# Kernel tuning notes

Measured on AMD Instinct MI355X. Metric: run time of the kernel, lower is better.

Reference implementation:

```python
import jax, jax.numpy as jnp
import numpy as np

B, L, D, C, H, NB = 2, 2048, 256, 8, 8, 2
S = 2                        # spatial coord dim of s
E = 2 * D - (C + 1)          # id-embedding width per D*2-(C+1)
FIN = 1 + S + E + C          # z + s + id-embed + conditionals
MAXLOC = 4096
DH = (2 * D) // H            # per-head dim


def _ln(x, sc, b):
    m = x.mean(-1, keepdims=True)
    v = ((x - m) ** 2).mean(-1, keepdims=True)
    return (x - m) * jax.lax.rsqrt(v + 1e-6) * sc + b


def setup_inputs() -> dict:
    key = jax.random.key(0)
    ks = iter(jax.random.split(key, 64))
    nrm = lambda shape: jax.random.normal(next(ks), shape, jnp.float32) * 0.02
    inp = {
        "z": jax.random.normal(next(ks), (B, L), jnp.float32),
        "conditionals": jax.random.normal(next(ks), (C,), jnp.float32),
        "s": jax.random.uniform(next(ks), (L, S), jnp.float32),
        "K": jax.random.uniform(next(ks), (L, L), jnp.float32),
        "embed": nrm((MAXLOC, E)),
        "W_in1": nrm((FIN, 4 * D)), "b_in1": jnp.zeros((4 * D,), jnp.float32),
        "W_in2": nrm((4 * D, D)), "b_in2": jnp.zeros((D,), jnp.float32),
        "bias_w": jnp.ones((NB,), jnp.float32), "bias_b": jnp.zeros((NB,), jnp.float32),
        "Wq": nrm((NB, D, 2 * D)), "bq": jnp.zeros((NB, 2 * D), jnp.float32),
        "Wk": nrm((NB, D, 2 * D)), "bk": jnp.zeros((NB, 2 * D), jnp.float32),
        "Wv": nrm((NB, D, 2 * D)), "bv": jnp.zeros((NB, 2 * D), jnp.float32),
        "Wo": nrm((NB, 2 * D, D)), "bo": jnp.zeros((NB, D), jnp.float32),
        "ln1_s": jnp.ones((NB, D), jnp.float32), "ln1_b": jnp.zeros((NB, D), jnp.float32),
        "ln2_s": jnp.ones((NB, D), jnp.float32), "ln2_b": jnp.zeros((NB, D), jnp.float32),
        "Wf1": nrm((NB, D, 4 * D)), "bf1": jnp.zeros((NB, 4 * D), jnp.float32),
        "Wf2": nrm((NB, 4 * D, D)), "bf2": jnp.zeros((NB, D), jnp.float32),
        "Wh1": nrm((D, 128)), "bh1": jnp.zeros((128,), jnp.float32),
        "Wh2": nrm((128, 1)), "bh2": jnp.zeros((1,), jnp.float32),
    }
    return inp


def reference(z, conditionals, s, K, embed, W_in1, b_in1, W_in2, b_in2,
              bias_w, bias_b, Wq, bq, Wk, bk, Wv, bv, Wo, bo,
              ln1_s, ln1_b, ln2_s, ln2_b, Wf1, bf1, Wf2, bf2,
              Wh1, bh1, Wh2, bh2):
    Bx, Lx = z.shape
    ids_e = embed[:Lx]  # ids = arange(L), so embedding lookup is a leading slice
    feats = jnp.concatenate([
        z[..., None],                                          # (B, L, 1)
        jnp.broadcast_to(s[None], (Bx, Lx, S)),                # (B, L, S)
        jnp.broadcast_to(ids_e[None], (Bx, Lx, E)),            # (B, L, E)
        jnp.broadcast_to(conditionals[None, None], (Bx, Lx, C)),  # cond_as_feats
    ], axis=-1)
    x = jax.nn.gelu(feats @ W_in1 + b_in1) @ W_in2 + b_in2     # (B, L, D)
    for i in range(NB):
        bias = bias_w[i] * K + bias_b[i]                        # learned scalar-affine kernel bias (L, L)
        h = _ln(x, ln1_s[i], ln1_b[i])
        q = (h @ Wq[i] + bq[i]).reshape(Bx, Lx, H, DH)
        k = (h @ Wk[i] + bk[i]).reshape(Bx, Lx, H, DH)
        v = (h @ Wv[i] + bv[i]).reshape(Bx, Lx, H, DH)
        scores = jnp.einsum('bqhd,bkhd->bhqk', q, k) / jnp.sqrt(jnp.float32(DH))
        scores = scores + bias[None, None]                      # broadcast over batch, heads
        a = jax.nn.softmax(scores, axis=-1)
        o = jnp.einsum('bhqk,bkhd->bqhd', a, v).reshape(Bx, Lx, 2 * D)
        x = x + (o @ Wo[i] + bo[i])
        h2 = _ln(x, ln2_s[i], ln2_b[i])
        x = x + jax.nn.gelu(h2 @ Wf1[i] + bf1[i]) @ Wf2[i] + bf2[i]
    return jax.nn.gelu(x @ Wh1 + bh1) @ Wh2 + bh2              # head MLP([128,1]) -> (B, L, 1)
```

## Files before the change

### kernel.cpp

```cpp
#include <hip/hip_runtime.h>
#include <math.h>

#define B_SZ 2
#define L_LEN 2048
#define D_MOD 256
#define H_HEADS 8
#define NB_BLK 2
#define S_SZ 2
#define E_SZ 503
#define C_SZ 8
#define FIN 514
#define FIN_PAD 576
#define LOG2E 1.44269504088896340736f
#define QSC (0.125f * LOG2E)

typedef short bf16x8 __attribute__((ext_vector_type(8)));
typedef float f32x4 __attribute__((ext_vector_type(4)));
typedef unsigned short u16x4 __attribute__((ext_vector_type(4)));
typedef unsigned short u16x8 __attribute__((ext_vector_type(8)));

#define OFF_IN1 0
#define OFF_IN2 589824
#define OFF_QKV 851968
#define OFF_O   1638400
#define OFF_F1  1900544
#define OFF_F2  2424832
#define OFF_H   2949120
#define WT_END  3047424

__device__ __forceinline__ unsigned short f2bf(float x) {
    unsigned u = __float_as_uint(x);
    u += 0x7FFFu + ((u >> 16) & 1u);
    return (unsigned short)(u >> 16);
}

__device__ __forceinline__ float bf2f(unsigned short h) {
    return __uint_as_float(((unsigned)h) << 16);
}

__device__ __forceinline__ float gelu_f(float x) {
    float x3 = x * x * x;
    return 0.5f * x * (1.0f + tanhf(0.7978845608028654f * (x + 0.044715f * x3)));
}

__device__ __forceinline__ void gll16(const void* g, void* l) {
    __builtin_amdgcn_global_load_lds(
        (const __attribute__((address_space(1))) unsigned int*)g,
        (__attribute__((address_space(3))) unsigned int*)l,
        16, 0, 0);
}

__global__ __launch_bounds__(256) void prep_kernel(
    const float* __restrict__ W_in1, const float* __restrict__ W_in2,
    const float* __restrict__ Wq, const float* __restrict__ Wk,
    const float* __restrict__ Wv, const float* __restrict__ Wo,
    const float* __restrict__ Wf1, const float* __restrict__ Wf2,
    const float* __restrict__ Wh1, const float* __restrict__ Kmat,
    const float* __restrict__ bias_w,
    const float* __restrict__ bq, const float* __restrict__ bk,
    const float* __restrict__ bv,
    const float* __restrict__ z, const float* __restrict__ s,
    const float* __restrict__ embed, const float* __restrict__ cond,
    unsigned short* __restrict__ wt, unsigned short* __restrict__ kmfrag,
    float* __restrict__ bqkv, unsigned short* __restrict__ feats)
{
    __shared__ unsigned short sT[64][65];
    int b = blockIdx.x;
    int t = threadIdx.x;

    if (b < 720) {
        const float* src; unsigned short* dst; int K, N, Kp, tile;
        float scale = 1.0f;
        if (b < 144)      { src = W_in1; dst = wt + OFF_IN1; K = 514;  N = 1024; Kp = 576;  tile = b; }
        else if (b < 208) { src = W_in2; dst = wt + OFF_IN2; K = 1024; N = 256;  Kp = 1024; tile = b - 144; }
        else if (b < 400) { int t2 = b - 208;
                            int sec = t2 >> 5; tile = t2 & 31;
                            int i = sec / 3, which = sec % 3;
                            const float* wsrc = which == 0 ? Wq : which == 1 ? Wk : Wv;
                            if (which == 0) scale = QSC;
                            src = wsrc + (size_t)i * 131072;
                            dst = wt + OFF_QKV + (size_t)i * 393216 + (size_t)which * 131072;
                            K = 256; N = 512; Kp = 256; }
        else if (b < 464) { int t2 = b - 400; int i = t2 >> 5; tile = t2 & 31;
                            src = Wo + (size_t)i * 131072; dst = wt + OFF_O + (size_t)i * 131072;
                            K = 512; N = 256; Kp = 512; }
        else if (b < 592) { int t2 = b - 464; int i = t2 >> 6; tile = t2 & 63;
                            src = Wf1 + (size_t)i * 262144; dst = wt + OFF_F1 + (size_t)i * 262144;
                            K = 256; N = 1024; Kp = 256; }
        else              { int t2 = b - 592; int i = t2 >> 6; tile = t2 & 63;
                            src = Wf2 + (size_t)i * 262144; dst = wt + OFF_F2 + (size_t)i * 262144;
                            K = 1024; N = 256; Kp = 1024; }

        int nt = N >> 6;
        int kt0 = (tile / nt) << 6;
        int nt0 = (tile % nt) << 6;
        #pragma unroll
        for (int p = 0; p < 4; p++) {
            int r = p * 16 + (t >> 4);
            int c = (t & 15) * 4;
            float4 v4 = make_float4(0.f, 0.f, 0.f, 0.f);
            if (kt0 + r < K) v4 = *(const float4*)(src + (size_t)(kt0 + r) * N + nt0 + c);
            sT[r][c + 0] = f2bf(v4.x * scale);
            sT[r][c + 1] = f2bf(v4.y * scale);
            sT[r][c + 2] = f2bf(v4.z * scale);
            sT[r][c + 3] = f2bf(v4.w * scale);
        }
        __syncthreads();
        int n = t >> 2, kq = (t & 3) * 16;
        u16x8 o0, o1;
        #pragma unroll
        for (int j = 0; j < 8; j++) {
            o0[j] = sT[kq + j][n];
            o1[j] = sT[kq + 8 + j][n];
        }
        unsigned short* dp = dst + (size_t)(nt0 + n) * Kp + kt0 + kq;
        *(u16x8*)(dp) = o0;
        *(u16x8*)(dp + 8) = o1;
    } else if (b < 1104) {
        int idx = (b - 720) * 256 + t;
        if (idx < 128 * 768) {
            int n = idx / 768, kk = idx % 768;
            int kz = kk & 255;
            float v = Wh1[(size_t)kz * 128 + n];
            unsigned short hi = f2bf(v);
            wt[OFF_H + idx] = (kk < 512) ? hi : f2bf(v - bf2f(hi));
        }
    } else if (b < 2128) {
        int tile = b - 1104;
        int kt = tile >> 5, qb = tile & 31;
        float s0 = bias_w[0] * LOG2E, s1 = bias_w[1] * LOG2E;
        int q0 = qb * 64 + ((t >> 6) << 4) + (((t >> 4) & 3) << 2);
        int k0 = kt * 64 + (t & 15);
        u16x8 a0, a1, b0, b1;
        #pragma unroll
        for (int c = 0; c < 4; c++)
            #pragma unroll
            for (int r = 0; r < 4; r++) {
                float v = Kmat[(size_t)(q0 + r) * L_LEN + k0 + c * 16];
                if (c < 2) { a0[c * 4 + r] = f2bf(v * s0); b0[c * 4 + r] = f2bf(v * s1); }
                else       { a1[(c - 2) * 4 + r] = f2bf(v * s0); b1[(c - 2) * 4 + r] = f2bf(v * s1); }
            }
        unsigned short* dp = kmfrag + (((size_t)(kt * 32 + qb)) * 256 + t) * 16;
        *(u16x8*)dp = a0;
        *(u16x8*)(dp + 8) = a1;
        unsigned short* dp1 = dp + ((size_t)1 << 22);
        *(u16x8*)dp1 = b0;
        *(u16x8*)(dp1 + 8) = b1;
    } else if (b < 2140) {
        int idx = (b - 2128) * 256 + t;
        if (idx < 2 * 1536) {
            int i = idx / 1536, c = idx % 1536;
            float v;
            if (c < 512)       v = bq[i * 512 + c] * QSC;
            else if (c < 1024) v = bk[i * 512 + c - 512];
            else               v = bv[i * 512 + c - 1024];
            bqkv[idx] = v;
        }
    } else {
        int idx = (b - 2140) * 256 + t;
        int l = idx / 144;
        int f0 = (idx % 144) * 4;
        u16x4 pk0, pk1;
        #pragma unroll
        for (int j = 0; j < 4; j++) {
            int f = f0 + j;
            float val;
            if (f >= 3 && f < 506)      val = embed[(size_t)l * E_SZ + (f - 3)];
            else if (f >= 1 && f < 3)   val = s[l * S_SZ + (f - 1)];
            else if (f >= 506 && f < FIN) val = cond[f - 506];
            else                        val = 0.0f;
            unsigned short hv = f2bf(val);
            pk0[j] = (f == 0) ? f2bf(z[l]) : hv;
            pk1[j] = (f == 0) ? f2bf(z[L_LEN + l]) : hv;
        }
        *(u16x4*)(feats + (size_t)l * FIN_PAD + f0) = pk0;
        *(u16x4*)(feats + (size_t)(L_LEN + l) * FIN_PAD + f0) = pk1;
    }
}

template<int ACT, int OMODE>
__global__ __launch_bounds__(256) void gemmW(
    const unsigned short* __restrict__ A, const unsigned short* __restrict__ Wt,
    const float* __restrict__ bias, unsigned short* __restrict__ Cb,
    unsigned short* __restrict__ Cbk, unsigned short* __restrict__ Cbv,
    int M, int N, int Kd, int lda)
{
    __shared__ unsigned short sA[2][64][64];
    __shared__ unsigned short sB[2][128][64];
    const int tid = threadIdx.x;
    const int l = tid & 63, w = tid >> 6;
    const int g = l >> 4, n16 = l & 15;
    const int wr = w >> 1, wc = w & 1;
    const int m0 = blockIdx.y * 64, n0 = blockIdx.x * 128;
    const int r8 = l >> 3;
    const int swz8 = ((l & 7) ^ r8) * 8;

    f32x4 acc[2][4];
    #pragma unroll
    for (int mi = 0; mi < 2; mi++)
        #pragma unroll
        for (int ni = 0; ni < 4; ni++)
            acc[mi][ni] = (f32x4){0.f, 0.f, 0.f, 0.f};

#define STAGEW(buf, k0)                                                         \
    do {                                                                        \
        _Pragma("unroll")                                                       \
        for (int p = 0; p < 2; p++) {                                           \
            int row = w * 16 + p * 8 + r8;                                      \
            gll16(A + (size_t)(m0 + row) * lda + (k0) + swz8,                   \
                  &sA[buf][w * 16 + p * 8][0]);                                 \
        }                                                                       \
        _Pragma("unroll")                                                       \
        for (int p = 0; p < 4; p++) {                                           \
            int row = w * 32 + p * 8 + r8;                                      \
            gll16(Wt + (size_t)(n0 + row) * Kd + (k0) + swz8,                   \
                  &sB[buf][w * 32 + p * 8][0]);                                 \
        }                                                                       \
    } while (0)

    STAGEW(0, 0);
    __syncthreads();

    int cur = 0;
    for (int k0 = 0; k0 < Kd; k0 += 64) {
        int nxt = cur ^ 1;
        if (k0 + 64 < Kd) STAGEW(nxt, k0 + 64);
        #pragma unroll
        for (int ks = 0; ks < 2; ks++) {
            bf16x8 af[2], bfr[4];
            #pragma unroll
            for (int mi = 0; mi < 2; mi++) {
                int row = wr * 32 + mi * 16 + n16;
                af[mi] = *(const bf16x8*)((const char*)&sA[cur][row][0]
                          + ((ks * 64 + g * 16) ^ ((n16 & 7) << 4)));
            }
            #pragma unroll
            for (int ni = 0; ni < 4; ni++) {
                int row = wc * 64 + ni * 16 + n16;
                bfr[ni] = *(const bf16x8*)((const char*)&sB[cur][row][0]
                          + ((ks * 64 + g * 16) ^ ((n16 & 7) << 4)));
            }
            #pragma unroll
            for (int mi = 0; mi < 2; mi++)
                #pragma unroll
                for (int ni = 0; ni < 4; ni++)
                    acc[mi][ni] = __builtin_amdgcn_mfma_f32_16x16x32_bf16(
                        af[mi], bfr[ni], acc[mi][ni], 0, 0, 0);
        }
        __syncthreads();
        cur = nxt;
    }
#undef STAGEW

    #pragma unroll
    for (int mi = 0; mi < 2; mi++) {
        #pragma unroll
        for (int ni = 0; ni < 4; ni++) {
            int col = n0 + wc * 64 + ni * 16 + n16;
            float bv = bias[col];
            #pragma unroll
            for (int r = 0; r < 4; r++) {
                int row = m0 + wr * 32 + mi * 16 + 4 * g + r;
                float val = acc[mi][ni][r] + bv;
                if (ACT == 1) val = gelu_f(val);
                if (OMODE == 1) {
                    Cb[(size_t)row * N + col] = f2bf(val);
                } else {
                    if (col < 1024) {
                        unsigned short* dst = (col < 512) ? Cb : Cbk;
                        dst[(size_t)row * 512 + (col & 511)] = f2bf(val);
                    } else {
                        Cbv[((size_t)(row >> 11) * 512 + (col - 1024)) * L_LEN + (row & (L_LEN - 1))] = f2bf(val);
                    }
                }
            }
        }
    }
}

template<int ACT, int OMODE, int BM>
__global__ __launch_bounds__(256) void gemm_bf16(
    const unsigned short* __restrict__ A, const unsigned short* __restrict__ Wt,
    const float* __restrict__ bias, float* __restrict__ Cf,
    unsigned short* __restrict__ Cb, int M, int N, int Kd, int lda)
{
    __shared__ unsigned short sA[2][BM][64];
    __shared__ unsigned short sB[2][64][64];
    const int tid = threadIdx.x;
    const int l = tid & 63, w = tid >> 6;
    const int g = l >> 4, n16 = l & 15;
    const int m0 = blockIdx.y * BM, n0 = blockIdx.x * 64;

    const int r8 = l >> 3;
    const int swz8 = ((l & 7) ^ r8) * 8;

    const int NMI = (BM == 64) ? 2 : 1;
    const int NNI = (BM == 16) ? 1 : 2;
    const int wr = w >> 1;
    const int wc = w & 1;

    f32x4 acc[2][2];
    #pragma unroll
    for (int mi = 0; mi < 2; mi++)
        #pragma unroll
        for (int ni = 0; ni < 2; ni++)
            acc[mi][ni] = (f32x4){0.f, 0.f, 0.f, 0.f};

#define STAGE(buf, k0)                                                          \
    do {                                                                        \
        if (BM == 64) {                                                         \
            _Pragma("unroll")                                                   \
            for (int p = 0; p < 2; p++) {                                       \
                int row = w * 16 + p * 8 + r8;                                  \
                gll16(A + (size_t)(m0 + row) * lda + (k0) + swz8,               \
                      &sA[buf][w * 16 + p * 8][0]);                             \
            }                                                                   \
        } else if (BM == 32) {                                                  \
            int row = w * 8 + r8;                                               \
            gll16(A + (size_t)(m0 + row) * lda + (k0) + swz8,                   \
                  &sA[buf][w * 8][0]);                                          \
        } else {                                                                \
            if (w < 2) {                                                        \
                int row = w * 8 + r8;                                           \
                gll16(A + (size_t)(m0 + row) * lda + (k0) + swz8,               \
                      &sA[buf][w * 8][0]);                                      \
            }                                                                   \
        }                                                                       \
        _Pragma("unroll")                                                       \
        for (int p = 0; p < 2; p++) {                                           \
            int row = w * 16 + p * 8 + r8;                                      \
            gll16(Wt + (size_t)(n0 + row) * Kd + (k0) + swz8,                   \
                  &sB[buf][w * 16 + p * 8][0]);                                 \
        }                                                                       \
    } while (0)

    STAGE(0, 0);
    __syncthreads();

    int cur = 0;
    for (int k0 = 0; k0 < Kd; k0 += 64) {
        int nxt = cur ^ 1;
        if (k0 + 64 < Kd) STAGE(nxt, k0 + 64);
        #pragma unroll
        for (int ks = 0; ks < 2; ks++) {
            bf16x8 af[2], bfr[2];
            #pragma unroll
            for (int mi = 0; mi < NMI; mi++) {
                int row = (BM == 64) ? (wr * 32 + mi * 16 + n16)
                        : (BM == 32) ? (wr * 16 + n16) : n16;
                af[mi] = *(const bf16x8*)((const char*)&sA[cur][row][0]
                          + ((ks * 64 + g * 16) ^ ((n16 & 7) << 4)));
            }
            #pragma unroll
            for (int ni = 0; ni < NNI; ni++) {
                int row = (BM == 16) ? (w * 16 + n16) : (wc * 32 + ni * 16 + n16);
                bfr[ni] = *(const bf16x8*)((const char*)&sB[cur][row][0]
                          + ((ks * 64 + g * 16) ^ ((n16 & 7) << 4)));
            }
            #pragma unroll
            for (int mi = 0; mi < NMI; mi++)
                #pragma unroll
                for (int ni = 0; ni < NNI; ni++)
                    acc[mi][ni] = __builtin_amdgcn_mfma_f32_16x16x32_bf16(
                        af[mi], bfr[ni], acc[mi][ni], 0, 0, 0);
        }
        __syncthreads();
        cur = nxt;
    }
#undef STAGE

    #pragma unroll
    for (int mi = 0; mi < NMI; mi++) {
        #pragma unroll
        for (int ni = 0; ni < NNI; ni++) {
            int col = (BM == 16) ? (n0 + w * 16 + n16)
                                 : (n0 + wc * 32 + ni * 16 + n16);
            float bv = bias[col];
            #pragma unroll
            for (int r = 0; r < 4; r++) {
                int row = (BM == 64) ? (m0 + wr * 32 + mi * 16 + 4 * g + r)
                        : (BM == 32) ? (m0 + wr * 16 + 4 * g + r)
                                     : (m0 + 4 * g + r);
                float val = acc[mi][ni][r] + bv;
                if (ACT == 1) val = gelu_f(val);
                if (OMODE == 0) {
                    Cf[(size_t)row * N + col] = val;
                } else if (OMODE == 1) {
                    Cb[(size_t)row * N + col] = f2bf(val);
                } else if (OMODE == 2) {
                    float* cp = Cf + (size_t)row * N + col;
                    *cp += val;
                } else if (OMODE == 5) {
                    float xnew = Cf[(size_t)row * N + col] + val;
                    unsigned short hi = f2bf(xnew);
                    unsigned short lo = f2bf(xnew - bf2f(hi));
                    unsigned short* orow = Cb + (size_t)row * 768;
                    orow[col] = hi;
                    orow[256 + col] = lo;
                    orow[512 + col] = hi;
                }
            }
        }
    }
}

__global__ __launch_bounds__(256) void ln_bf16(
    const float* __restrict__ x, const float* __restrict__ sc,
    const float* __restrict__ bi, unsigned short* __restrict__ out)
{
    int wave = threadIdx.x >> 6, lane = threadIdx.x & 63;
    int row = blockIdx.x * 4 + wave;
    const float* xr = x + (size_t)row * D_MOD;
    float4 v = *(const float4*)(xr + lane * 4);
    float s1 = v.x + v.y + v.z + v.w;
    float s2 = v.x * v.x + v.y * v.y + v.z * v.z + v.w * v.w;
    #pragma unroll
    for (int off = 1; off < 64; off <<= 1) {
        s1 += __shfl_xor(s1, off);
        s2 += __shfl_xor(s2, off);
    }
    float mean = s1 * (1.0f / 256.0f);
    float var = s2 * (1.0f / 256.0f) - mean * mean;
    float rs = rsqrtf(var + 1e-6f);
    float4 scv = *(const float4*)(sc + lane * 4);
    float4 bv  = *(const float4*)(bi + lane * 4);
    u16x4 o4;
    o4[0] = f2bf((v.x - mean) * rs * scv.x + bv.x);
    o4[1] = f2bf((v.y - mean) * rs * scv.y + bv.y);
    o4[2] = f2bf((v.z - mean) * rs * scv.z + bv.z);
    o4[3] = f2bf((v.w - mean) * rs * scv.w + bv.w);
    *(u16x4*)(out + (size_t)row * D_MOD + lane * 4) = o4;
}

__global__ __launch_bounds__(256, 2) void attn_mfma(
    const unsigned short* __restrict__ q, const unsigned short* __restrict__ k,
    const unsigned short* __restrict__ vt, const unsigned short* __restrict__ kmf,
    unsigned short* __restrict__ o)
{
    __shared__ unsigned short sK[2][64][64];
    __shared__ unsigned short sV[2][64][64];
    __shared__ unsigned short sP[4][16][72];

    const int tid = threadIdx.x;
    const int l = tid & 63, w = tid >> 6;
    const int g = l >> 4, n16 = l & 15;
    const int qblk = blockIdx.x * 64, hh = blockIdx.y, b = blockIdx.z;

    const int r8 = l >> 3;
    const int swz8 = ((l & 7) ^ r8) * 8;

    bf16x8 qf[2];
    {
        const unsigned short* qp = q + (size_t)(b * L_LEN + qblk + w * 16 + n16) * 512 + hh * 64;
        qf[0] = *(const bf16x8*)(qp + g * 8);
        qf[1] = *(const bf16x8*)(qp + 32 + g * 8);
    }
    bf16x8 onesf;
    #pragma unroll
    for (int j = 0; j < 8; j++) onesf[j] = (short)0x3F80;

    f32x4 o_acc[4];
    #pragma unroll
    for (int c = 0; c < 4; c++) o_acc[c] = (f32x4){0.f, 0.f, 0.f, 0.f};
    f32x4 l_acc = (f32x4){0.f, 0.f, 0.f, 0.f};

    const unsigned short* kbase = k + (size_t)b * L_LEN * 512 + hh * 64;
    const unsigned short* vbase = vt + ((size_t)b * 512 + hh * 64) * L_LEN;
    const unsigned short* kmbase = kmf + ((size_t)blockIdx.x * 256 + tid) * 16;

    #pragma unroll
    for (int p = 0; p < 2; p++) {
        int row = w * 16 + p * 8 + r8;
        gll16(kbase + (size_t)row * 512 + swz8, &sK[0][w * 16 + p * 8][0]);
        gll16(vbase + (size_t)row * L_LEN + swz8, &sV[0][w * 16 + p * 8][0]);
    }
    u16x8 kmC0 = *(const u16x8*)kmbase;
    u16x8 kmC1 = *(const u16x8*)(kmbase + 8);
    __syncthreads();

    int cur = 0;
    for (int kt = 0; kt < L_LEN / 64; kt++) {
        const int nb = cur ^ 1;
        const int kblk2 = (kt + 1) << 6;
        u16x8 kmN0 = kmC0, kmN1 = kmC1;
        if (kt + 1 < L_LEN / 64) {
            #pragma unroll
            for (int p = 0; p < 2; p++) {
                int row = w * 16 + p * 8 + r8;
                gll16(kbase + (size_t)(kblk2 + row) * 512 + swz8, &sK[nb][w * 16 + p * 8][0]);
                gll16(vbase + (size_t)row * L_LEN + kblk2 + swz8, &sV[nb][w * 16 + p * 8][0]);
            }
            const unsigned short* kp2 = kmbase + (size_t)(kt + 1) * 131072;
            kmN0 = *(const u16x8*)kp2;
            kmN1 = *(const u16x8*)(kp2 + 8);
        }
        f32x4 sacc[4];
        #pragma unroll
        for (int c = 0; c < 4; c++)
            #pragma unroll
            for (int r = 0; r < 4; r++)
                sacc[c][r] = bf2f((unsigned short)(c < 2 ? kmC0[c * 4 + r] : kmC1[(c - 2) * 4 + r]));
        __builtin_amdgcn_s_setprio(1);
        #pragma unroll
        for (int ks = 0; ks < 2; ks++)
            #pragma unroll
            for (int c = 0; c < 4; c++) {
                int row = c * 16 + n16;
                bf16x8 kf = *(const bf16x8*)((const char*)&sK[cur][row][0]
                             + ((ks * 64 + g * 16) ^ ((n16 & 7) << 4)));
                sacc[c] = __builtin_amdgcn_mfma_f32_16x16x32_bf16(qf[ks], kf, sacc[c], 0, 0, 0);
            }
        __builtin_amdgcn_s_setprio(0);
        float p[4][4];
        #pragma unroll
        for (int r = 0; r < 4; r++)
            #pragma unroll
            for (int c = 0; c < 4; c++)
                p[r][c] = __builtin_amdgcn_exp2f(sacc[c][r]);
        #pragma unroll
        for (int r = 0; r < 4; r++)
            #pragma unroll
            for (int c = 0; c < 4; c++)
                sP[w][4 * g + r][c * 16 + n16] = f2bf(p[r][c]);
        __builtin_amdgcn_s_setprio(1);
        #pragma unroll
        for (int ks = 0; ks < 2; ks++) {
            bf16x8 pf = *(const bf16x8*)&sP[w][n16][ks * 32 + g * 8];
            l_acc = __builtin_amdgcn_mfma_f32_16x16x32_bf16(pf, onesf, l_acc, 0, 0, 0);
            #pragma unroll
            for (int c = 0; c < 4; c++) {
                int row = c * 16 + n16;
                bf16x8 vf = *(const bf16x8*)((const char*)&sV[cur][row][0]
                             + ((ks * 64 + g * 16) ^ ((n16 & 7) << 4)));
                o_acc[c] = __builtin_amdgcn_mfma_f32_16x16x32_bf16(pf, vf, o_acc[c], 0, 0, 0);
            }
        }
        __builtin_amdgcn_s_setprio(0);
        __syncthreads();
        cur = nb;
        kmC0 = kmN0;
        kmC1 = kmN1;
    }

    float inv[4];
    #pragma unroll
    for (int r = 0; r < 4; r++) inv[r] = 1.0f / l_acc[r];
    #pragma unroll
    for (int c = 0; c < 4; c++)
        #pragma unroll
        for (int r = 0; r < 4; r++)
            o[(size_t)(b * L_LEN + qblk + w * 16 + 4 * g + r) * 512 + hh * 64 + c * 16 + n16]
                = f2bf(o_acc[c][r] * inv[r]);
}

__global__ __launch_bounds__(256) void hsum_kernel(
    const unsigned short* __restrict__ hb, const float* __restrict__ Wh2,
    const float* __restrict__ bh2, float* __restrict__ out)
{
    int wave = threadIdx.x >> 6, lane = threadIdx.x & 63;
    int row = blockIdx.x * 4 + wave;
    unsigned v = *(const unsigned*)(hb + (size_t)row * 128 + lane * 2);
    float v0 = __uint_as_float((v & 0xFFFFu) << 16);
    float v1 = __uint_as_float(v & 0xFFFF0000u);
    float val = v0 * Wh2[lane * 2] + v1 * Wh2[lane * 2 + 1];
    #pragma unroll
    for (int off = 1; off < 64; off <<= 1)
        val += __shfl_xor(val, off);
    if (lane == 0) out[row] = val + bh2[0];
}

extern "C" void kernel_launch(void* const* d_in, const int* in_sizes, int n_in,
                              void* d_out, int out_size, void* d_ws, size_t ws_size,
                              hipStream_t stream)
{
    const float* z      = (const float*)d_in[0];
    const float* cond   = (const float*)d_in[1];
    const float* s      = (const float*)d_in[2];
    const float* Kmat   = (const float*)d_in[3];
    const float* embed  = (const float*)d_in[4];
    const float* W_in1  = (const float*)d_in[5];
    const float* b_in1  = (const float*)d_in[6];
    const float* W_in2  = (const float*)d_in[7];
    const float* b_in2  = (const float*)d_in[8];
    const float* bias_w = (const float*)d_in[9];
    const float* bias_b = (const float*)d_in[10];
    const float* Wq     = (const float*)d_in[11];
    const float* bq     = (const float*)d_in[12];
    const float* Wk     = (const float*)d_in[13];
    const float* bk     = (const float*)d_in[14];
    const float* Wv     = (const float*)d_in[15];
    const float* bv     = (const float*)d_in[16];
    const float* Wo     = (const float*)d_in[17];
    const float* bo     = (const float*)d_in[18];
    const float* ln1_s  = (const float*)d_in[19];
    const float* ln1_b  = (const float*)d_in[20];
    const float* ln2_s  = (const float*)d_in[21];
    const float* ln2_b  = (const float*)d_in[22];
    const float* Wf1    = (const float*)d_in[23];
    const float* bf1    = (const float*)d_in[24];
    const float* Wf2    = (const float*)d_in[25];
    const float* bf2    = (const float*)d_in[26];
    const float* Wh1    = (const float*)d_in[27];
    const float* bh1    = (const float*)d_in[28];
    const float* Wh2    = (const float*)d_in[29];
    const float* bh2    = (const float*)d_in[30];
    float* out = (float*)d_out;
    (void)bias_b;

    const int M = B_SZ * L_LEN;
    char* base = (char*)d_ws;
    unsigned short* feats = (unsigned short*)base;
    float* x = (float*)(base + (size_t)M * FIN_PAD * 2);
    unsigned short* h    = (unsigned short*)((char*)x + (size_t)M * D_MOD * 4);
    unsigned short* hid1 = h    + (size_t)M * D_MOD;
    unsigned short* qb   = hid1 + (size_t)M * 1024;
    unsigned short* kb2  = qb   + (size_t)M * 512;
    unsigned short* vtb  = kb2  + (size_t)M * 512;
    unsigned short* ob   = vtb  + (size_t)M * 512;
    unsigned short* wt   = ob   + (size_t)M * 512;
    float* bqkv          = (float*)(wt + WT_END);
    unsigned short* kmfrag = (unsigned short*)(bqkv + 2 * 1536);

    prep_kernel<<<dim3(3292), dim3(256), 0, stream>>>(
        W_in1, W_in2, Wq, Wk, Wv, Wo, Wf1, Wf2, Wh1, Kmat, bias_w,
        bq, bk, bv, z, s, embed, cond, wt, kmfrag, bqkv, feats);

    gemmW<1, 1><<<dim3(8, 64), 256, 0, stream>>>(feats, wt + OFF_IN1, b_in1, hid1, nullptr, nullptr, M, 1024, FIN_PAD, FIN_PAD);
    gemm_bf16<0, 0, 16><<<dim3(4, 256), 256, 0, stream>>>(hid1, wt + OFF_IN2, b_in2, x, nullptr, M, 256, 1024, 1024);

    for (int i = 0; i < NB_BLK; i++) {
        ln_bf16<<<dim3(M / 4), 256, 0, stream>>>(x, ln1_s + i * D_MOD, ln1_b + i * D_MOD, h);
        gemmW<0, 4><<<dim3(12, 64), 256, 0, stream>>>(h, wt + OFF_QKV + (size_t)i * 393216, bqkv + i * 1536, qb, kb2, vtb, M, 1536, 256, 256);
        attn_mfma<<<dim3(L_LEN / 64, H_HEADS, B_SZ), 256, 0, stream>>>(qb, kb2, vtb, kmfrag + ((size_t)i << 22), ob);
        gemm_bf16<0, 2, 16><<<dim3(4, 256), 256, 0, stream>>>(ob, wt + OFF_O + (size_t)i * 131072, bo + i * D_MOD, x, nullptr, M, 256, 512, 512);
        ln_bf16<<<dim3(M / 4), 256, 0, stream>>>(x, ln2_s + i * D_MOD, ln2_b + i * D_MOD, h);
        gemmW<1, 1><<<dim3(8, 64), 256, 0, stream>>>(h, wt + OFF_F1 + (size_t)i * 262144, bf1 + i * 1024, hid1, nullptr, nullptr, M, 1024, 256, 256);
        if (i == 0)
            gemm_bf16<0, 2, 16><<<dim3(4, 256), 256, 0, stream>>>(hid1, wt + OFF_F2 + (size_t)i * 262144, bf2 + i * D_MOD, x, nullptr, M, 256, 1024, 1024);
        else
            gemm_bf16<0, 5, 16><<<dim3(4, 256), 256, 0, stream>>>(hid1, wt + OFF_F2 + (size_t)i * 262144, bf2 + i * D_MOD, x, qb, M, 256, 1024, 1024);
    }
    gemm_bf16<1, 1, 16><<<dim3(2, 256), 256, 0, stream>>>(qb, wt + OFF_H, bh1, nullptr, ob, M, 128, 768, 768);
    hsum_kernel<<<dim3(M / 4), 256, 0, stream>>>(ob, Wh2, bh2, out);
}
```

Measured before the change: 232.8 us.

## Remap attention blocks per XCD and fuse head MLP into one kernel

```diff
diff --git a/kernel.cpp b/kernel.cpp
--- a/kernel.cpp
+++ b/kernel.cpp
@@ -444,7 +444,12 @@
     const int tid = threadIdx.x;
     const int l = tid & 63, w = tid >> 6;
     const int g = l >> 4, n16 = l & 15;
-    const int qblk = blockIdx.x * 64, hh = blockIdx.y, b = blockIdx.z;
+
+    const int id = blockIdx.x;
+    const int xcd = id & 7, rr2 = id >> 3;
+    const int panel = xcd * 2 + (rr2 & 1);
+    const int qi = rr2 >> 1;
+    const int qblk = qi * 64, hh = panel & 7, b = panel >> 3;
 
     const int r8 = l >> 3;
     const int swz8 = ((l & 7) ^ r8) * 8;
@@ -466,7 +471,7 @@
 
     const unsigned short* kbase = k + (size_t)b * L_LEN * 512 + hh * 64;
     const unsigned short* vbase = vt + ((size_t)b * 512 + hh * 64) * L_LEN;
-    const unsigned short* kmbase = kmf + ((size_t)blockIdx.x * 256 + tid) * 16;
+    const unsigned short* kmbase = kmf + ((size_t)qi * 256 + tid) * 16;
 
     #pragma unroll
     for (int p = 0; p < 2; p++) {
@@ -553,20 +558,85 @@
                 = f2bf(o_acc[c][r] * inv[r]);
 }
 
-__global__ __launch_bounds__(256) void hsum_kernel(
-    const unsigned short* __restrict__ hb, const float* __restrict__ Wh2,
+__global__ __launch_bounds__(256) void head_kernel(
+    const unsigned short* __restrict__ A, const unsigned short* __restrict__ Wt,
+    const float* __restrict__ bh1, const float* __restrict__ Wh2,
     const float* __restrict__ bh2, float* __restrict__ out)
 {
-    int wave = threadIdx.x >> 6, lane = threadIdx.x & 63;
-    int row = blockIdx.x * 4 + wave;
-    unsigned v = *(const unsigned*)(hb + (size_t)row * 128 + lane * 2);
-    float v0 = __uint_as_float((v & 0xFFFFu) << 16);
-    float v1 = __uint_as_float(v & 0xFFFF0000u);
-    float val = v0 * Wh2[lane * 2] + v1 * Wh2[lane * 2 + 1];
-    #pragma unroll
-    for (int off = 1; off < 64; off <<= 1)
-        val += __shfl_xor(val, off);
-    if (lane == 0) out[row] = val + bh2[0];
+    __shared__ unsigned short sA[2][16][64];
+    __shared__ unsigned short sB[2][128][64];
+    __shared__ float sRed[4][16];
+    const int tid = threadIdx.x;
+    const int l = tid & 63, w = tid >> 6;
+    const int g = l >> 4, n16 = l & 15;
+    const int m0 = blockIdx.x * 16;
+    const int r8 = l >> 3;
+    const int swz8 = ((l & 7) ^ r8) * 8;
+
+    f32x4 acc[2];
+    acc[0] = (f32x4){0.f, 0.f, 0.f, 0.f};
+    acc[1] = (f32x4){0.f, 0.f, 0.f, 0.f};
+
+#define HSTAGE(buf, k0)                                                         \
+    do {                                                                        \
+        if (w < 2) {                                                            \
+            int row = w * 8 + r8;                                               \
+            gll16(A + (size_t)(m0 + row) * 768 + (k0) + swz8,                   \
+                  &sA[buf][w * 8][0]);                                          \
+        }                                                                       \
+        _Pragma("unroll")                                                       \
+        for (int p = 0; p < 4; p++) {                                           \
+            int row = w * 32 + p * 8 + r8;                                      \
+            gll16(Wt + (size_t)row * 768 + (k0) + swz8,                         \
+                  &sB[buf][w * 32 + p * 8][0]);                                 \
+        }                                                                       \
+    } while (0)
+
+    HSTAGE(0, 0);
+    __syncthreads();
+
+    int cur = 0;
+    for (int k0 = 0; k0 < 768; k0 += 64) {
+        int nxt = cur ^ 1;
+        if (k0 + 64 < 768) HSTAGE(nxt, k0 + 64);
+        #pragma unroll
+        for (int ks = 0; ks < 2; ks++) {
+            bf16x8 af = *(const bf16x8*)((const char*)&sA[cur][n16][0]
+                         + ((ks * 64 + g * 16) ^ ((n16 & 7) << 4)));
+            #pragma unroll
+            for (int ni = 0; ni < 2; ni++) {
+                int row = w * 32 + ni * 16 + n16;
+                bf16x8 bfr = *(const bf16x8*)((const char*)&sB[cur][row][0]
+                              + ((ks * 64 + g * 16) ^ ((n16 & 7) << 4)));
+                acc[ni] = __builtin_amdgcn_mfma_f32_16x16x32_bf16(af, bfr, acc[ni], 0, 0, 0);
+            }
+        }
+        __syncthreads();
+        cur = nxt;
+    }
+#undef HSTAGE
+
+    float s[4];
+    #pragma unroll
+    for (int r = 0; r < 4; r++) {
+        s[r] = 0.f;
+        #pragma unroll
+        for (int ni = 0; ni < 2; ni++) {
+            int col = w * 32 + ni * 16 + n16;
+            s[r] += gelu_f(acc[ni][r] + bh1[col]) * Wh2[col];
+        }
+        s[r] += __shfl_xor(s[r], 1);
+        s[r] += __shfl_xor(s[r], 2);
+        s[r] += __shfl_xor(s[r], 4);
+        s[r] += __shfl_xor(s[r], 8);
+    }
+    if (n16 == 0) {
+        #pragma unroll
+        for (int r = 0; r < 4; r++) sRed[w][4 * g + r] = s[r];
+    }
+    __syncthreads();
+    if (tid < 16)
+        out[m0 + tid] = sRed[0][tid] + sRed[1][tid] + sRed[2][tid] + sRed[3][tid] + bh2[0];
 }
 
 extern "C" void kernel_launch(void* const* d_in, const int* in_sizes, int n_in,
@@ -631,7 +701,7 @@
     for (int i = 0; i < NB_BLK; i++) {
         ln_bf16<<<dim3(M / 4), 256, 0, stream>>>(x, ln1_s + i * D_MOD, ln1_b + i * D_MOD, h);
         gemmW<0, 4><<<dim3(12, 64), 256, 0, stream>>>(h, wt + OFF_QKV + (size_t)i * 393216, bqkv + i * 1536, qb, kb2, vtb, M, 1536, 256, 256);
-        attn_mfma<<<dim3(L_LEN / 64, H_HEADS, B_SZ), 256, 0, stream>>>(qb, kb2, vtb, kmfrag + ((size_t)i << 22), ob);
+        attn_mfma<<<dim3(512), 256, 0, stream>>>(qb, kb2, vtb, kmfrag + ((size_t)i << 22), ob);
         gemm_bf16<0, 2, 16><<<dim3(4, 256), 256, 0, stream>>>(ob, wt + OFF_O + (size_t)i * 131072, bo + i * D_MOD, x, nullptr, M, 256, 512, 512);
         ln_bf16<<<dim3(M / 4), 256, 0, stream>>>(x, ln2_s + i * D_MOD, ln2_b + i * D_MOD, h);
         gemmW<1, 1><<<dim3(8, 64), 256, 0, stream>>>(h, wt + OFF_F1 + (size_t)i * 262144, bf1 + i * 1024, hid1, nullptr, nullptr, M, 1024, 256, 256);
@@ -640,6 +710,5 @@
         else
             gemm_bf16<0, 5, 16><<<dim3(4, 256), 256, 0, stream>>>(hid1, wt + OFF_F2 + (size_t)i * 262144, bf2 + i * D_MOD, x, qb, M, 256, 1024, 1024);
     }
-    gemm_bf16<1, 1, 16><<<dim3(2, 256), 256, 0, stream>>>(qb, wt + OFF_H, bh1, nullptr, ob, M, 128, 768, 768);
-    hsum_kernel<<<dim3(M / 4), 256, 0, stream>>>(ob, Wh2, bh2, out);
-}
+    head_kernel<<<dim3(256), 256, 0, stream>>>(qb, wt + OFF_H, bh1, Wh2, bh2, out);
+}
```

Result: no change. 234.3 us (+0.7%).
